# Optimization experiments

Measured on AMD Instinct MI355X. Metric: run time of the kernel, lower is better.

Reference implementation:

```python
import jax, jax.numpy as jnp
import numpy as np

N = 100_000   # nodes
E = 2_400_000 # edges (before self-loops)
H = 32        # hidden_size == num_features
NEG_SLOPE = 0.2


def setup_inputs() -> dict:
    key = jax.random.key(0)
    ks = jax.random.split(key, 16)
    rn = lambda k, s, sc=1.0: (jax.random.normal(k, s, dtype=jnp.float32) * sc)
    return {
        'x': rn(ks[0], (N, H)),
        'edge_index': jax.random.randint(ks[1], (2, E), 0, N, dtype=jnp.int32),
        'conv_W': rn(ks[2], (H, H), 0.1),
        'conv_att_src': rn(ks[3], (H,), 0.1),
        'conv_att_dst': rn(ks[4], (H,), 0.1),
        'conv_bias': jnp.zeros((H,), jnp.float32),
        'gru_Wih0': rn(ks[5], (3 * H, H), 0.1),
        'gru_Whh0': rn(ks[6], (3 * H, H), 0.1),
        'gru_bih0': rn(ks[7], (3 * H,), 0.1),
        'gru_bhh0': rn(ks[8], (3 * H,), 0.1),
        'gru_Wih1': rn(ks[9], (3 * H, H), 0.1),
        'gru_Whh1': rn(ks[10], (3 * H, H), 0.1),
        'gru_bih1': rn(ks[11], (3 * H,), 0.1),
        'gru_bhh1': rn(ks[12], (3 * H,), 0.1),
        'lin_W': rn(ks[13], (1, H), 0.1),
        'lin_b': jnp.zeros((1,), jnp.float32),
    }


def _gat_conv(x, edge_index, W, att_src, att_dst, bias):
    # PyG GATConv, heads=1, concat=True, add_self_loops=True.
    h = x @ W.T                                     # [N, H]
    loop = jnp.arange(N, dtype=edge_index.dtype)
    src = jnp.concatenate([edge_index[0], loop])    # [E+N]
    dst = jnp.concatenate([edge_index[1], loop])
    a_s = h @ att_src                               # [N]
    a_d = h @ att_dst
    e = jax.nn.leaky_relu(a_s[src] + a_d[dst], NEG_SLOPE)  # [E+N]
    # segment softmax over incoming edges of each dst node
    m = jax.ops.segment_max(e, dst, num_segments=N)        # each node has a self-loop
    p = jnp.exp(e - m[dst])
    denom = jax.ops.segment_sum(p, dst, num_segments=N)
    alpha = p / denom[dst]                                  # [E+N]
    out = jax.ops.segment_sum(alpha[:, None] * h[src], dst, num_segments=N)
    return out + bias


def _gru_cell_zero_h(x, Wih, Whh, bih, bhh):
    # Single GRU step with h_prev = 0 (seq_len == 1, h0 zeros). Gate order: r, z, n.
    gi = x @ Wih.T + bih                    # [N, 3H]
    h0 = jnp.zeros_like(x)
    gh = h0 @ Whh.T + bhh                   # [N, 3H] (Whh contributes zero)
    i_r, i_z, i_n = jnp.split(gi, 3, axis=-1)
    h_r, h_z, h_n = jnp.split(gh, 3, axis=-1)
    r = jax.nn.sigmoid(i_r + h_r)
    z = jax.nn.sigmoid(i_z + h_z)
    n = jnp.tanh(i_n + r * h_n)
    return (1.0 - z) * n                    # + z * h0, h0 = 0


def reference(x, edge_index, conv_W, conv_att_src, conv_att_dst, conv_bias,
              gru_Wih0, gru_Whh0, gru_bih0, gru_bhh0,
              gru_Wih1, gru_Whh1, gru_bih1, gru_bhh1,
              lin_W, lin_b):
    h = jax.nn.relu(x)
    h = _gat_conv(h, edge_index, conv_W, conv_att_src, conv_att_dst, conv_bias)
    h = _gru_cell_zero_h(h, gru_Wih0, gru_Whh0, gru_bih0, gru_bhh0)
    h = _gru_cell_zero_h(h, gru_Wih1, gru_Whh1, gru_bih1, gru_bhh1)
    h = _gat_conv(h, edge_index, conv_W, conv_att_src, conv_att_dst, conv_bias)
    return h @ lin_W.T + lin_b              # [N, 1]
```

## Files before the change

kernel.cpp:

```cpp
#include <hip/hip_runtime.h>
#include <hip/hip_fp16.h>
#include <math.h>

#define Hd 32
#define NEG 0.2f
#define BSH 8
#define BN (1 << BSH)
#define CHUNK 8192
#define NBUCK_MAX 512
#define WP 36

__device__ __forceinline__ float lrelu(float x) { return x > 0.f ? x : NEG * x; }
__device__ __forceinline__ float fsigm(float x) { return 1.f / (1.f + __expf(-x)); }
__device__ __forceinline__ float ftanh(float x) { return 1.f - 2.f / (__expf(2.f * x) + 1.f); }


__global__ void k_histb(const int* __restrict__ dst, int* __restrict__ counts,
                        int E, int nchunk, int nbuck)
{
    __shared__ int hh[NBUCK_MAX];
    int c = blockIdx.x, t = threadIdx.x;
    for (int i = t; i < nbuck; i += 256) hh[i] = 0;
    __syncthreads();
    int beg = c * CHUNK, end = min(beg + CHUNK, E);
    for (int k = beg + t; k < end; k += 256) atomicAdd(&hh[dst[k] >> BSH], 1);
    __syncthreads();
    for (int i = t; i < nbuck; i += 256) counts[i * nchunk + c] = hh[i];
}

__global__ void k_scan1(const int* __restrict__ in, int* __restrict__ bsum, int L)
{
    __shared__ int sd[256];
    int t = threadIdx.x;
    int i = blockIdx.x * 256 + t;
    sd[t] = (i < L) ? in[i] : 0;
    __syncthreads();
    for (int s = 128; s > 0; s >>= 1) {
        if (t < s) sd[t] += sd[t + s];
        __syncthreads();
    }
    if (t == 0) bsum[blockIdx.x] = sd[0];
}

__global__ void k_scan2(int* __restrict__ bsum, int nb)
{
    __shared__ int sd[1024];
    int t = threadIdx.x;
    int v = (t < nb) ? bsum[t] : 0;
    sd[t] = v;
    __syncthreads();
    for (int o = 1; o < 1024; o <<= 1) {
        int x = (t >= o) ? sd[t - o] : 0;
        __syncthreads();
        sd[t] += x;
        __syncthreads();
    }
    if (t < nb) bsum[t] = sd[t] - v;
}

__global__ void k_scan3(const int* __restrict__ in, const int* __restrict__ bsum,
                        int* __restrict__ out, int L)
{
    __shared__ int sd[256];
    int t = threadIdx.x;
    int i = blockIdx.x * 256 + t;
    int v = (i < L) ? in[i] : 0;
    sd[t] = v;
    __syncthreads();
    for (int o = 1; o < 256; o <<= 1) {
        int x = (t >= o) ? sd[t - o] : 0;
        __syncthreads();
        sd[t] += x;
        __syncthreads();
    }
    if (i < L) out[i] = bsum[blockIdx.x] + sd[t] - v;
}

__global__ void k_scatterb(const int* __restrict__ src, const int* __restrict__ dst,
                           const int* __restrict__ cstart, unsigned* __restrict__ tmp,
                           int E, int nchunk, int nbuck)
{
    __shared__ int cur[NBUCK_MAX];
    int c = blockIdx.x, t = threadIdx.x;
    for (int i = t; i < nbuck; i += 256) cur[i] = cstart[i * nchunk + c];
    __syncthreads();
    int beg = c * CHUNK, end = min(beg + CHUNK, E);
    for (int k = beg + t; k < end; k += 256) {
        int d = dst[k];
        int pos = atomicAdd(&cur[d >> BSH], 1);
        tmp[pos] = ((unsigned)(d & (BN - 1)) << 17) | (unsigned)src[k];
    }
}

__global__ void k_place2(const unsigned* __restrict__ tmp, const int* __restrict__ cstart,
                         int* __restrict__ csr, int* __restrict__ off_g, int* __restrict__ cnt_g,
                         int N, int E, int nchunk, int nbuck)
{
    __shared__ int lcnt[BN];
    __shared__ int lscan[BN];
    __shared__ int lcur[BN];
    int b = blockIdx.x, t = threadIdx.x;
    int bstart = cstart[b * nchunk];
    int bend = (b + 1 < nbuck) ? cstart[(b + 1) * nchunk] : E;
    lcnt[t] = 0;
    __syncthreads();
    for (int k = bstart + t; k < bend; k += 256)
        atomicAdd(&lcnt[tmp[k] >> 17], 1);
    __syncthreads();
    int c = lcnt[t];
    lscan[t] = c;
    __syncthreads();
    for (int o = 1; o < 256; o <<= 1) {
        int x = (t >= o) ? lscan[t - o] : 0;
        __syncthreads();
        lscan[t] += x;
        __syncthreads();
    }
    int o0 = bstart + lscan[t] - c;
    int node = (b << BSH) + t;
    lcur[t] = o0;
    if (node < N) { off_g[node] = o0; cnt_g[node] = c; }
    __syncthreads();
    for (int k = bstart + t; k < bend; k += 256) {
        unsigned v = tmp[k];
        int pos = atomicAdd(&lcur[v >> 17], 1);
        csr[pos] = (int)(v & 0x1FFFFu);
    }
}


template<bool RELU>
__global__ void k_node_proj(const float* __restrict__ x, const float* __restrict__ W,
                            const float* __restrict__ att_s, const float* __restrict__ att_d,
                            __half* __restrict__ h16, float* __restrict__ as_, float* __restrict__ ad_,
                            int N)
{
    __shared__ float Wl[Hd][Hd + 1];
    __shared__ float xr[8][Hd];
    int tid = threadIdx.x;
    for (int i = tid; i < Hd * Hd; i += 256) Wl[i >> 5][i & 31] = W[i];
    int li = tid >> 5, j = tid & 31;
    float asj = att_s[j], adj = att_d[j];
    __syncthreads();
#pragma unroll 1
    for (int tile = 0; tile < 4; tile++) {
        int node = (blockIdx.x * 4 + tile) * 8 + li;
        float v = 0.f;
        if (node < N) v = x[(size_t)node * Hd + j];
        if (RELU) v = fmaxf(v, 0.f);
        xr[li][j] = v;
        float a = 0.f;
#pragma unroll
        for (int k = 0; k < Hd; k++) a += xr[li][k] * Wl[j][k];
        float s = a * asj, d = a * adj;
#pragma unroll
        for (int m = 16; m > 0; m >>= 1) { s += __shfl_xor(s, m, 32); d += __shfl_xor(d, m, 32); }
        if (node < N) {
            h16[(size_t)node * Hd + j] = __float2half(a);
            if (j == 0) { as_[node] = s; ad_[node] = d; }
        }
    }
}

template<int MODE>
__global__ void k_gather(const __half* __restrict__ h16, const float* __restrict__ as_,
                         const float* __restrict__ ad_, const int* __restrict__ cnt,
                         const int* __restrict__ off, const int* __restrict__ csr_src,
                         const float* __restrict__ bias, const float* __restrict__ linW,
                         const float* __restrict__ linb, float* __restrict__ out, int N)
{
    int idx = blockIdx.x * 256 + threadIdx.x;
    int n = idx >> 5;
    if (n >= N) return;
    int j = idx & 31;
    int g = j >> 3, q = j & 7;
    int beg = off[n], deg = cnt[n];
    float adn = ad_[n];

    float denp = 0.f;
    float4 acc = make_float4(0.f, 0.f, 0.f, 0.f);

    for (int c = 0; c < deg; c += 32) {
        int k = c + j;
        int sj = n; float pj = 0.f;
        if (k < deg) { sj = csr_src[beg + k]; pj = __expf(lrelu(as_[sj] + adn)); }
        denp += pj;
#pragma unroll
        for (int t = 0; t < 8; t++) {
            int lsrc = t * 4 + g;
            float p = __shfl(pj, lsrc, 32);
            int   s = __shfl(sj, lsrc, 32);
            uint2 rv = ((const uint2*)(h16 + (size_t)s * Hd))[q];
            float2 f01 = __half22float2(*reinterpret_cast<const __half2*>(&rv.x));
            float2 f23 = __half22float2(*reinterpret_cast<const __half2*>(&rv.y));
            acc.x = fmaf(p, f01.x, acc.x);
            acc.y = fmaf(p, f01.y, acc.y);
            acc.z = fmaf(p, f23.x, acc.z);
            acc.w = fmaf(p, f23.y, acc.w);
        }
    }

    float pself = __expf(lrelu(as_[n] + adn));
    if (g == 0) {
        uint2 rv = ((const uint2*)(h16 + (size_t)n * Hd))[q];
        float2 f01 = __half22float2(*reinterpret_cast<const __half2*>(&rv.x));
        float2 f23 = __half22float2(*reinterpret_cast<const __half2*>(&rv.y));
        acc.x = fmaf(pself, f01.x, acc.x);
        acc.y = fmaf(pself, f01.y, acc.y);
        acc.z = fmaf(pself, f23.x, acc.z);
        acc.w = fmaf(pself, f23.y, acc.w);
    }
#pragma unroll
    for (int o = 16; o > 0; o >>= 1) denp += __shfl_xor(denp, o, 32);
    float den = denp + pself;
#pragma unroll
    for (int o = 8; o <= 16; o <<= 1) {
        acc.x += __shfl_xor(acc.x, o, 32);
        acc.y += __shfl_xor(acc.y, o, 32);
        acc.z += __shfl_xor(acc.z, o, 32);
        acc.w += __shfl_xor(acc.w, o, 32);
    }
    float inv = 1.f / den;
    float4 b4 = ((const float4*)bias)[q];
    if (MODE == 0) {
        if (g == 0) {
            float4 o4;
            o4.x = fmaf(acc.x, inv, b4.x);
            o4.y = fmaf(acc.y, inv, b4.y);
            o4.z = fmaf(acc.z, inv, b4.z);
            o4.w = fmaf(acc.w, inv, b4.w);
            ((float4*)(out + (size_t)n * Hd))[q] = o4;
        }
    } else {
        float4 w4 = ((const float4*)linW)[q];
        float s = fmaf(acc.x, inv, b4.x) * w4.x
                + fmaf(acc.y, inv, b4.y) * w4.y
                + fmaf(acc.z, inv, b4.z) * w4.z
                + fmaf(acc.w, inv, b4.w) * w4.w;
#pragma unroll
        for (int o = 1; o <= 4; o <<= 1) s += __shfl_xor(s, o, 32);
        if (j == 0) out[n] = s + linb[0];
    }
}

__global__ __launch_bounds__(256) void k_gru2(
    const float* __restrict__ in,
    const float* __restrict__ Wih0, const float* __restrict__ bih0, const float* __restrict__ bhh0,
    const float* __restrict__ Wih1, const float* __restrict__ bih1, const float* __restrict__ bhh1,
    float* __restrict__ out, int N)
{
    __shared__ __align__(16) float W0l[96 * WP];
    __shared__ __align__(16) float W1l[96 * WP];
    __shared__ __align__(16) float rows[8][4][Hd];
    int tid = threadIdx.x;
    for (int i = tid; i < 96 * Hd; i += 256) {
        int r = i >> 5, k = i & 31;
        W0l[r * WP + k] = Wih0[i];
        W1l[r * WP + k] = Wih1[i];
    }
    int g = tid >> 5, j = tid & 31;
    int node0 = blockIdx.x * 32 + g * 4;
#pragma unroll
    for (int i = 0; i < 4; i++) {
        int node = node0 + i;
        rows[g][i][j] = (node < N) ? in[(size_t)node * Hd + j] : 0.f;
    }
    float br0 = bih0[j], bz0 = bih0[32 + j], bn0 = bih0[64 + j];
    float hr0 = bhh0[j], hz0 = bhh0[32 + j], hn0 = bhh0[64 + j];
    float br1 = bih1[j], bz1 = bih1[32 + j], bn1 = bih1[64 + j];
    float hr1 = bhh1[j], hz1 = bhh1[32 + j], hn1 = bhh1[64 + j];
    __syncthreads();

    float ar[4], az[4], an[4];
#pragma unroll
    for (int i = 0; i < 4; i++) { ar[i] = br0; az[i] = bz0; an[i] = bn0; }
#pragma unroll 2
    for (int k4 = 0; k4 < 8; k4++) {
        float4 wr = *(const float4*)&W0l[(j     ) * WP + k4 * 4];
        float4 wz = *(const float4*)&W0l[(32 + j) * WP + k4 * 4];
        float4 wn = *(const float4*)&W0l[(64 + j) * WP + k4 * 4];
#pragma unroll
        for (int i = 0; i < 4; i++) {
            float4 xv = *(const float4*)&rows[g][i][k4 * 4];
            ar[i] = fmaf(xv.x, wr.x, ar[i]); ar[i] = fmaf(xv.y, wr.y, ar[i]);
            ar[i] = fmaf(xv.z, wr.z, ar[i]); ar[i] = fmaf(xv.w, wr.w, ar[i]);
            az[i] = fmaf(xv.x, wz.x, az[i]); az[i] = fmaf(xv.y, wz.y, az[i]);
            az[i] = fmaf(xv.z, wz.z, az[i]); az[i] = fmaf(xv.w, wz.w, az[i]);
            an[i] = fmaf(xv.x, wn.x, an[i]); an[i] = fmaf(xv.y, wn.y, an[i]);
            an[i] = fmaf(xv.z, wn.z, an[i]); an[i] = fmaf(xv.w, wn.w, an[i]);
        }
    }
#pragma unroll
    for (int i = 0; i < 4; i++) {
        float r = fsigm(ar[i] + hr0);
        float z = fsigm(az[i] + hz0);
        float t = ftanh(an[i] + r * hn0);
        rows[g][i][j] = (1.f - z) * t;
    }

#pragma unroll
    for (int i = 0; i < 4; i++) { ar[i] = br1; az[i] = bz1; an[i] = bn1; }
#pragma unroll 2
    for (int k4 = 0; k4 < 8; k4++) {
        float4 wr = *(const float4*)&W1l[(j     ) * WP + k4 * 4];
        float4 wz = *(const float4*)&W1l[(32 + j) * WP + k4 * 4];
        float4 wn = *(const float4*)&W1l[(64 + j) * WP + k4 * 4];
#pragma unroll
        for (int i = 0; i < 4; i++) {
            float4 xv = *(const float4*)&rows[g][i][k4 * 4];
            ar[i] = fmaf(xv.x, wr.x, ar[i]); ar[i] = fmaf(xv.y, wr.y, ar[i]);
            ar[i] = fmaf(xv.z, wr.z, ar[i]); ar[i] = fmaf(xv.w, wr.w, ar[i]);
            az[i] = fmaf(xv.x, wz.x, az[i]); az[i] = fmaf(xv.y, wz.y, az[i]);
            az[i] = fmaf(xv.z, wz.z, az[i]); az[i] = fmaf(xv.w, wz.w, az[i]);
            an[i] = fmaf(xv.x, wn.x, an[i]); an[i] = fmaf(xv.y, wn.y, an[i]);
            an[i] = fmaf(xv.z, wn.z, an[i]); an[i] = fmaf(xv.w, wn.w, an[i]);
        }
    }
#pragma unroll
    for (int i = 0; i < 4; i++) {
        float r = fsigm(ar[i] + hr1);
        float z = fsigm(az[i] + hz1);
        float t = ftanh(an[i] + r * hn1);
        int node = node0 + i;
        if (node < N) out[(size_t)node * Hd + j] = (1.f - z) * t;
    }
}

extern "C" void kernel_launch(void* const* d_in, const int* in_sizes, int n_in,
                              void* d_out, int out_size, void* d_ws, size_t ws_size,
                              hipStream_t stream)
{
    const float* x    = (const float*)d_in[0];
    const int*   ei   = (const int*)d_in[1];
    const float* W    = (const float*)d_in[2];
    const float* atts = (const float*)d_in[3];
    const float* attd = (const float*)d_in[4];
    const float* bias = (const float*)d_in[5];
    const float* Wih0 = (const float*)d_in[6];
    const float* bih0 = (const float*)d_in[8];
    const float* bhh0 = (const float*)d_in[9];
    const float* Wih1 = (const float*)d_in[10];
    const float* bih1 = (const float*)d_in[12];
    const float* bhh1 = (const float*)d_in[13];
    const float* linW = (const float*)d_in[14];
    const float* linb = (const float*)d_in[15];

    int N = in_sizes[0] / Hd;
    int E = in_sizes[1] / 2;
    const int* src = ei;
    const int* dst = ei + E;
    int nbuck = (N + BN - 1) >> BSH;
    int nchunk = (E + CHUNK - 1) / CHUNK;
    int L = nbuck * nchunk;
    int nbL = (L + 255) / 256;

    __half* h16  = (__half*)d_ws;
    float* base  = (float*)d_ws;
    float* gat   = base + (size_t)N * Hd;
    float* h2    = gat  + (size_t)N * Hd;
    float* as_   = h2   + (size_t)N * Hd;
    float* ad_   = as_ + N;
    int*   cnt   = (int*)(ad_ + N);
    int*   off   = cnt + N;
    int*   counts= off + N;
    int*   cstart= counts + L;
    int*   bsum  = cstart + L;
    int*   csr   = bsum + 1024;
    unsigned* tmp = (unsigned*)gat;

    dim3 blk(256);
    dim3 g_proj((N + 31) / 32);
    dim3 g_nf((N * Hd + 255) / 256);
    dim3 g_gru((N + 31) / 32);

    hipLaunchKernelGGL(k_histb, dim3(nchunk), blk, 0, stream, dst, counts, E, nchunk, nbuck);
    hipLaunchKernelGGL(k_scan1, dim3(nbL), blk, 0, stream, counts, bsum, L);
    hipLaunchKernelGGL(k_scan2, dim3(1), dim3(1024), 0, stream, bsum, nbL);
    hipLaunchKernelGGL(k_scan3, dim3(nbL), blk, 0, stream, counts, bsum, cstart, L);
    hipLaunchKernelGGL(k_scatterb, dim3(nchunk), blk, 0, stream, src, dst, cstart, tmp, E, nchunk, nbuck);
    hipLaunchKernelGGL(k_place2, dim3(nbuck), blk, 0, stream, tmp, cstart, csr, off, cnt, N, E, nchunk, nbuck);

    hipLaunchKernelGGL((k_node_proj<true>), g_proj, blk, 0, stream, x, W, atts, attd, h16, as_, ad_, N);
    hipLaunchKernelGGL((k_gather<0>), g_nf, blk, 0, stream, h16, as_, ad_, cnt, off, csr, bias, linW, linb, gat, N);
    hipLaunchKernelGGL(k_gru2, g_gru, blk, 0, stream, gat, Wih0, bih0, bhh0, Wih1, bih1, bhh1, h2, N);

    hipLaunchKernelGGL((k_node_proj<false>), g_proj, blk, 0, stream, h2, W, atts, attd, h16, as_, ad_, N);
    hipLaunchKernelGGL((k_gather<1>), g_nf, blk, 0, stream, h16, as_, ad_, cnt, off, csr, bias, linW, linb, (float*)d_out, N);
}
```

Measured before the change: 214.0 us.

## Stage bucket scatter in shared memory for coalesced writes, halve chunk size

The bucket scatter kernel now first places each chunk's edges into a shared-memory buffer ordered by bucket, using a local prefix scan of the per-bucket counts. It then writes them out contiguously to the global temp array, so each bucket's run is written in order instead of as scattered single-word stores. CHUNK is halved to 4096 so the 64-bit shared buffer (32KB) fits, which doubles the number of chunks and the size of the count/cstart arrays. The extra cost is a block scan, a second pass over the chunk and more histogram/scan work, in exchange for more coalesced global writes.

```diff
diff --git a/kernel.cpp b/kernel.cpp
--- a/kernel.cpp
+++ b/kernel.cpp
@@ -6,7 +6,7 @@
 #define NEG 0.2f
 #define BSH 8
 #define BN (1 << BSH)
-#define CHUNK 8192
+#define CHUNK 4096
 #define NBUCK_MAX 512
 #define WP 36
 
@@ -77,18 +77,47 @@
 }
 
 __global__ void k_scatterb(const int* __restrict__ src, const int* __restrict__ dst,
-                           const int* __restrict__ cstart, unsigned* __restrict__ tmp,
-                           int E, int nchunk, int nbuck)
-{
+                           const int* __restrict__ counts, const int* __restrict__ cstart,
+                           unsigned* __restrict__ tmp, int E, int nchunk, int nbuck)
+{
+    __shared__ unsigned long long ebuf[CHUNK];
+    __shared__ int lstart[NBUCK_MAX];
+    __shared__ int gbase[NBUCK_MAX];
     __shared__ int cur[NBUCK_MAX];
+    __shared__ int lscan[256];
     int c = blockIdx.x, t = threadIdx.x;
-    for (int i = t; i < nbuck; i += 256) cur[i] = cstart[i * nchunk + c];
+    int b0 = 2 * t, b1 = b0 + 1;
+    int n0 = (b0 < nbuck) ? counts[(size_t)b0 * nchunk + c] : 0;
+    int n1 = (b1 < nbuck) ? counts[(size_t)b1 * nchunk + c] : 0;
+    if (b0 < nbuck) gbase[b0] = cstart[(size_t)b0 * nchunk + c];
+    if (b1 < nbuck) gbase[b1] = cstart[(size_t)b1 * nchunk + c];
+    int pair = n0 + n1;
+    lscan[t] = pair;
+    __syncthreads();
+    for (int o = 1; o < 256; o <<= 1) {
+        int x = (t >= o) ? lscan[t - o] : 0;
+        __syncthreads();
+        lscan[t] += x;
+        __syncthreads();
+    }
+    int excl = lscan[t] - pair;
+    if (b0 < nbuck) { lstart[b0] = excl;      cur[b0] = excl; }
+    if (b1 < nbuck) { lstart[b1] = excl + n0; cur[b1] = excl + n0; }
     __syncthreads();
     int beg = c * CHUNK, end = min(beg + CHUNK, E);
     for (int k = beg + t; k < end; k += 256) {
         int d = dst[k];
         int pos = atomicAdd(&cur[d >> BSH], 1);
-        tmp[pos] = ((unsigned)(d & (BN - 1)) << 17) | (unsigned)src[k];
+        ebuf[pos] = ((unsigned long long)(unsigned)d << 17) | (unsigned)src[k];
+    }
+    __syncthreads();
+    int csize = end - beg;
+    for (int i = t; i < csize; i += 256) {
+        unsigned long long v = ebuf[i];
+        int d = (int)(v >> 17);
+        int b = d >> BSH;
+        tmp[gbase[b] + (i - lstart[b])] =
+            ((unsigned)(d & (BN - 1)) << 17) | (unsigned)(v & 0x1FFFFu);
     }
 }
 
@@ -100,8 +129,8 @@
     __shared__ int lscan[BN];
     __shared__ int lcur[BN];
     int b = blockIdx.x, t = threadIdx.x;
-    int bstart = cstart[b * nchunk];
-    int bend = (b + 1 < nbuck) ? cstart[(b + 1) * nchunk] : E;
+    int bstart = cstart[(size_t)b * nchunk];
+    int bend = (b + 1 < nbuck) ? cstart[(size_t)(b + 1) * nchunk] : E;
     lcnt[t] = 0;
     __syncthreads();
     for (int k = bstart + t; k < bend; k += 256)
@@ -377,7 +406,7 @@
     hipLaunchKernelGGL(k_scan1, dim3(nbL), blk, 0, stream, counts, bsum, L);
     hipLaunchKernelGGL(k_scan2, dim3(1), dim3(1024), 0, stream, bsum, nbL);
     hipLaunchKernelGGL(k_scan3, dim3(nbL), blk, 0, stream, counts, bsum, cstart, L);
-    hipLaunchKernelGGL(k_scatterb, dim3(nchunk), blk, 0, stream, src, dst, cstart, tmp, E, nchunk, nbuck);
+    hipLaunchKernelGGL(k_scatterb, dim3(nchunk), blk, 0, stream, src, dst, counts, cstart, tmp, E, nchunk, nbuck);
     hipLaunchKernelGGL(k_place2, dim3(nbuck), blk, 0, stream, tmp, cstart, csr, off, cnt, N, E, nchunk, nbuck);
 
     hipLaunchKernelGGL((k_node_proj<true>), g_proj, blk, 0, stream, x, W, atts, attd, h16, as_, ad_, N);
```

After: 202.8 us. -5.3%, faster.
